# Kernel tuning notes

Measured on AMD Instinct MI355X. Metric: run time of the kernel, lower is better.

Reference implementation:

```python
import jax, jax.numpy as jnp
import numpy as np

D_MODEL = 512
D_STATE = 64
D_CONV = 4
EXPAND = 2
D_INNER = EXPAND * D_MODEL          # 1024
DT_RANK = (D_MODEL + 15) // 16      # 32 (ceil(d_model/16), standard Mamba)
B, L = 2, 1024
EPS = 1e-6


def setup_inputs() -> dict:
    key = jax.random.key(0)
    ks = jax.random.split(key, 12)
    s = 0.02
    p = {}
    p["x"] = jax.random.normal(ks[0], (B, L, D_MODEL), jnp.float32)
    # shared _Mamba params (share_dir=True)
    p["W_in"] = jax.random.normal(ks[1], (2 * D_INNER, D_MODEL), jnp.float32) * s
    p["conv_w"] = jax.random.normal(ks[2], (D_INNER, 1, D_CONV), jnp.float32) * s
    p["conv_b"] = jnp.zeros((D_INNER,), jnp.float32)
    p["W_xproj"] = jax.random.normal(ks[3], (DT_RANK + 2 * D_STATE, D_INNER), jnp.float32) * s
    p["W_dt"] = jax.random.normal(ks[4], (D_INNER, DT_RANK), jnp.float32) * s
    p["b_dt"] = jax.random.uniform(ks[5], (D_INNER,), jnp.float32, -4.0, -2.0)  # small dt after softplus
    p["A_log"] = jnp.log(jnp.broadcast_to(jnp.arange(1, D_STATE + 1, dtype=jnp.float32), (D_INNER, D_STATE)))
    p["Dskip"] = jnp.ones((D_INNER,), jnp.float32)
    p["W_out"] = jax.random.normal(ks[6], (D_MODEL, D_INNER), jnp.float32) * s
    # block params
    p["norm_in_w"] = jnp.ones((D_MODEL,), jnp.float32)
    p["fuse_W"] = jax.random.normal(ks[7], (2 * D_MODEL, 2 * D_MODEL), jnp.float32) * s
    p["fuse_b"] = jnp.zeros((2 * D_MODEL,), jnp.float32)
    p["ff_W1"] = jax.random.normal(ks[8], (4 * D_MODEL, D_MODEL), jnp.float32) * s
    p["ff_W2"] = jax.random.normal(ks[9], (D_MODEL, 4 * D_MODEL), jnp.float32) * s
    p["norm_out_w"] = jnp.ones((D_MODEL,), jnp.float32)
    return p


def _rmsnorm(x, w):
    x32 = x.astype(jnp.float32)
    var = jnp.mean(x32 * x32, axis=-1, keepdims=True)
    return (w * (x32 * jax.lax.rsqrt(var + EPS))).astype(x.dtype)


def _mamba(h, W_in, conv_w, conv_b, W_xproj, W_dt, b_dt, A_log, Dskip, W_out):
    # h: [B, L, D_MODEL]
    xz = jnp.einsum('bld,ed->ble', h, W_in)           # [B,L,2*D_INNER]
    u, z = jnp.split(xz, 2, axis=-1)
    # depthwise causal conv over time
    uc = jnp.transpose(u, (0, 2, 1))                  # [B,D_INNER,L]
    uc = jax.lax.conv_general_dilated(uc, conv_w, (1,), [(D_CONV - 1, 0)],
                                      feature_group_count=D_INNER)
    u = jax.nn.silu(jnp.transpose(uc, (0, 2, 1)) + conv_b)  # [B,L,D_INNER]
    x_dbl = jnp.einsum('bld,ed->ble', u, W_xproj)     # [B,L,DT_RANK+2N]
    dt = jax.nn.softplus(jnp.einsum('blr,dr->bld', x_dbl[..., :DT_RANK], W_dt) + b_dt)  # [B,L,D_INNER]
    Bm = x_dbl[..., DT_RANK:DT_RANK + D_STATE]        # [B,L,N]
    Cm = x_dbl[..., DT_RANK + D_STATE:]               # [B,L,N]
    A = -jnp.exp(A_log)                               # [D_INNER,N]

    def step(s, inp):
        dt_t, B_t, C_t, u_t = inp                     # [B,Din],[B,N],[B,N],[B,Din]
        dA = jnp.exp(dt_t[..., None] * A)             # [B,Din,N]
        s = s * dA + (dt_t * u_t)[..., None] * B_t[:, None, :]
        y_t = jnp.einsum('bdn,bn->bd', s, C_t)
        return s, y_t

    s0 = jnp.zeros((h.shape[0], D_INNER, D_STATE), h.dtype)
    xs = (jnp.moveaxis(dt, 1, 0), jnp.moveaxis(Bm, 1, 0),
          jnp.moveaxis(Cm, 1, 0), jnp.moveaxis(u, 1, 0))
    _, ys = jax.lax.scan(step, s0, xs)                # [L,B,D_INNER]
    y = jnp.moveaxis(ys, 0, 1) + u * Dskip
    return jnp.einsum('bld,ed->ble', y * jax.nn.silu(z), W_out)


def reference(x, W_in, conv_w, conv_b, W_xproj, W_dt, b_dt, A_log, Dskip, W_out,
              norm_in_w, fuse_W, fuse_b, ff_W1, ff_W2, norm_out_w):
    h = _rmsnorm(x, norm_in_w)
    mam = lambda t: _mamba(t, W_in, conv_w, conv_b, W_xproj, W_dt, b_dt, A_log, Dskip, W_out)
    hf = mam(h)
    hb = jnp.flip(mam(jnp.flip(h, axis=1)), axis=1)   # shared params (share_dir=True)
    hcat = jnp.concatenate([hf, hb], axis=-1)         # [B,L,2D]
    uv = jnp.einsum('ble,fe->blf', hcat, fuse_W) + fuse_b
    ug, vg = jnp.split(uv, 2, axis=-1)
    h = ug * jax.nn.sigmoid(vg)                        # GLU fuse
    ff = jnp.einsum('bld,fd->blf', jax.nn.silu(h), ff_W1)
    ff = jnp.einsum('blf,df->bld', jax.nn.silu(ff), ff_W2)
    y = x + ff                                         # dropout=0 (eval)
    return _rmsnorm(y, norm_out_w)
```

## Files before the change

### kernel.cpp

```cpp
#include <hip/hip_runtime.h>
#include <math.h>

#define L_SEQ 1024
#define NC 64
#define CL 16

typedef unsigned short ushort_t;
typedef __attribute__((ext_vector_type(8))) short bf16x8_t;
typedef __attribute__((ext_vector_type(4))) float f32x4_t;
typedef __attribute__((ext_vector_type(2))) float f32x2_t;

__device__ __forceinline__ float sigmoidf_(float x){ return 1.f/(1.f+__expf(-x)); }
__device__ __forceinline__ float siluf_(float x){ return x*sigmoidf_(x); }
__device__ __forceinline__ float softplusf_(float x){ return (x>20.f)?x:log1pf(__expf(x)); }
__device__ __forceinline__ ushort_t f2bf(float f){
  union { float f; unsigned u; } a; a.f = f;
  unsigned u = a.u;
  unsigned r = (u + 0x7fffu + ((u >> 16) & 1u)) >> 16;
  return (ushort_t)r;
}
__device__ __forceinline__ float bf2f(ushort_t v){
  union { unsigned u; float f; } a; a.u = ((unsigned)v) << 16; return a.f;
}
__device__ __forceinline__ ushort_t f2h(float f){
  union { _Float16 h; ushort_t u; } c; c.h = (_Float16)f; return c.u;
}
__device__ __forceinline__ float h2f(ushort_t u){
  union { ushort_t u; _Float16 h; } c; c.u = u; return (float)c.h;
}

__global__ __launch_bounds__(256) void cast_all_weights(
    ushort_t* __restrict__ dst,
    const float* __restrict__ W_in, const float* __restrict__ W_xproj,
    const float* __restrict__ W_dt, const float* __restrict__ W_out,
    const float* __restrict__ fuse_W, const float* __restrict__ ff_W1,
    const float* __restrict__ ff_W2)
{
  int i = blockIdx.x*256 + threadIdx.x;
  if (i >= 4947968) return;
  float v;
  if (i < 1048576) v = W_in[i];
  else if (i < 1245184) { int j = i-1048576; v = (j < 163840) ? W_xproj[j] : 0.f; }
  else if (i < 1277952) v = W_dt[i-1245184];
  else if (i < 1802240) v = W_out[i-1277952];
  else if (i < 2850816) v = fuse_W[i-1802240];
  else if (i < 3899392) v = ff_W1[i-2850816];
  else v = ff_W2[i-3899392];
  dst[i] = f2bf(v);
}

__global__ __launch_bounds__(256) void rmsnorm_kernel(
    float* __restrict__ outf, ushort_t* __restrict__ outb,
    const float* __restrict__ in, const float* __restrict__ res,
    const float* __restrict__ w)
{
  int row = blockIdx.x, tid = threadIdx.x;
  size_t base = (size_t)row*512;
  float v0 = in[base+tid], v1 = in[base+tid+256];
  if (res) { v0 += res[base+tid]; v1 += res[base+tid+256]; }
  float ss = v0*v0 + v1*v1;
  #pragma unroll
  for (int off=32; off>0; off>>=1) ss += __shfl_down(ss, off, 64);
  __shared__ float red[4];
  int wv = tid>>6, ln = tid&63;
  if (ln==0) red[wv]=ss;
  __syncthreads();
  float tot = red[0]+red[1]+red[2]+red[3];
  float sc = rsqrtf(tot*(1.f/512.f) + 1e-6f);
  float o0 = w[tid]*v0*sc, o1 = w[tid+256]*v1*sc;
  if (outb) { outb[base+tid] = f2bf(o0); outb[base+tid+256] = f2bf(o1); }
  else      { outf[base+tid] = o0;       outf[base+tid+256] = o1; }
}

template<int TM, int TN>
__global__ __launch_bounds__(256) void mfma_gemm(
    const ushort_t* __restrict__ A, int lda,
    const ushort_t* __restrict__ W, int ldw,
    float* __restrict__ Cf, ushort_t* __restrict__ Cb, int ldc,
    int N, int K, const float* __restrict__ bias, int act, int dsplit,
    ushort_t* __restrict__ Pr, ushort_t* __restrict__ Pdtu,
    const ushort_t* __restrict__ Pu)
{
  constexpr int BM = 32*TM, BN = 32*TN;
  constexpr int NSEG = (BM + BN) / 16;
  __shared__ ushort_t As[BM*32];
  __shared__ ushort_t Bs[BN*32];
  const int tid = threadIdx.x;
  const int wid = tid >> 6, lane = tid & 63;
  const int wm = (wid & 1) * (16*TM);
  const int wn = (wid >> 1) * (16*TN);
  const int row0 = blockIdx.y * BM;
  const int col0 = blockIdx.x * BN;
  const int qd = lane >> 4, lr = lane & 15;
  const int seg_row = lane >> 2;
  const int seg_col = (lane & 3) * 8;

  f32x4_t acc[TM][TN];
  #pragma unroll
  for (int i=0;i<TM;++i)
    #pragma unroll
    for (int j=0;j<TN;++j) acc[i][j] = (f32x4_t)(0.f);

  for (int k0 = 0; k0 < K; k0 += 32) {
    #pragma unroll
    for (int ss = 0; ss < NSEG/4; ++ss) {
      int s = wid + ss*4;
      bool isA = (s < BM/16);
      int r = isA ? s*16 : (s - BM/16)*16;
      const ushort_t* gp = isA
          ? (A + (size_t)(row0 + r + seg_row)*lda + k0 + seg_col)
          : (W + (size_t)(col0 + r + seg_row)*ldw + k0 + seg_col);
      ushort_t* lp = (isA ? As : Bs) + r*32;
      __builtin_amdgcn_global_load_lds(
          (const __attribute__((address_space(1))) void*)gp,
          (__attribute__((address_space(3))) void*)lp, 16, 0, 0);
    }
    __syncthreads();
    bf16x8_t af[TM], bfv[TN];
    #pragma unroll
    for (int mi=0; mi<TM; ++mi)
      af[mi] = *(const bf16x8_t*)(As + (wm + mi*16 + lr)*32 + qd*8);
    #pragma unroll
    for (int ni=0; ni<TN; ++ni)
      bfv[ni] = *(const bf16x8_t*)(Bs + (wn + ni*16 + lr)*32 + qd*8);
    #pragma unroll
    for (int mi=0; mi<TM; ++mi)
      #pragma unroll
      for (int ni=0; ni<TN; ++ni)
        acc[mi][ni] = __builtin_amdgcn_mfma_f32_16x16x32_bf16(af[mi], bfv[ni], acc[mi][ni], 0, 0, 0);
    __syncthreads();
  }

  #pragma unroll
  for (int ni=0; ni<TN; ++ni) {
    int col = col0 + wn + ni*16 + lr;
    if (col >= N) continue;
    float bv = bias ? bias[col] : 0.f;
    #pragma unroll
    for (int mi=0; mi<TM; ++mi) {
      #pragma unroll
      for (int r=0; r<4; ++r) {
        int row = row0 + wm + mi*16 + qd*4 + r;
        float v = acc[mi][ni][r] + bv;
        if (act == 1) v = softplusf_(v);
        else if (act == 2) v = siluf_(v);
        size_t off;
        if (dsplit && row >= 2048) off = (size_t)(row-2048)*ldc + 512 + col;
        else                       off = (size_t)row*ldc + col;
        if (Pr) {
          float uu = bf2f(Pu[off]);
          Pr[off]   = f2h(__expf(-v));
          Pdtu[off] = f2bf(v*uu);
        } else {
          if (Cf) Cf[off] = v;
          if (Cb) Cb[off] = f2bf(v);
        }
      }
    }
  }
}

__global__ __launch_bounds__(256) void conv_silu_kernel(
    ushort_t* __restrict__ ubf, const ushort_t* __restrict__ xzb,
    const float* __restrict__ conv_w, const float* __restrict__ conv_b)
{
  size_t gid = (size_t)blockIdx.x*256 + threadIdx.x;
  int d   = gid & 1023;
  int l   = (gid >> 10) & 1023;
  int b   = (gid >> 20) & 1;
  int dir = (int)(gid >> 21);
  const float4 wv = ((const float4*)conv_w)[d];
  const float wk[4] = {wv.x, wv.y, wv.z, wv.w};
  const ushort_t* xp = xzb + (size_t)b*L_SEQ*2048 + d;
  float acc = conv_b[d];
  if (dir == 0) {
    #pragma unroll
    for (int k=0;k<4;++k){ int ll=l-3+k; if(ll>=0) acc += bf2f(xp[(size_t)ll*2048])*wk[k]; }
  } else {
    #pragma unroll
    for (int k=0;k<4;++k){ int ll=l+3-k; if(ll<L_SEQ) acc += bf2f(xp[(size_t)ll*2048])*wk[k]; }
  }
  size_t oidx = (size_t)dir*2097152 + ((size_t)b*L_SEQ + l)*1024 + d;
  ubf[oidx] = f2bf(siluf_(acc));
}


__global__ __launch_bounds__(256) void scan_pass1(
    const ushort_t* __restrict__ rb, const ushort_t* __restrict__ dtub,
    const float* __restrict__ xdbl,
    float* __restrict__ prch, ushort_t* __restrict__ qbuf)
{
  __shared__ float bst[CL*64];
  int tid = threadIdx.x;
  int w = tid >> 6, lane = tid & 63;
  int dblk = blockIdx.x, c = blockIdx.y, sd = blockIdx.z;
  int b = sd>>1, dir = sd&1;
  int d = (dblk<<6) + lane;
  int n0 = w*16;
  size_t dbo = (size_t)dir*2097152 + (size_t)b*1048576;
  const ushort_t* rp  = rb   + dbo;
  const ushort_t* dup = dtub + dbo;
  const float* xd = xdbl + (size_t)dir*327680 + (size_t)b*163840;
  int l0c = c*CL;
  {
    int e = tid;
    int li = e >> 4, fo = (e & 15) << 2;
    int l = dir ? (L_SEQ-1-(l0c+li)) : (l0c+li);
    *(float4*)(bst + li*64 + fo) = *(const float4*)(xd + (size_t)l*160 + 32 + fo);
  }
  __syncthreads();
  f32x2_t s2[8];
  #pragma unroll
  for (int n=0;n<8;++n) s2[n]=(f32x2_t)(0.f);
  float pr = 1.f;
  int l0 = dir ? (L_SEQ-1-l0c) : l0c;
  float rv_n = h2f(rp[(size_t)l0*1024 + d]);
  float du_n = bf2f(dup[(size_t)l0*1024 + d]);
  #pragma unroll 1
  for (int i=0;i<CL;++i) {
    float rv = rv_n, du = du_n;
    if (i+1 < CL) {
      int l2 = dir ? (l0-i-1) : (l0+i+1);
      rv_n = h2f(rp[(size_t)l2*1024 + d]);
      du_n = bf2f(dup[(size_t)l2*1024 + d]);
    }
    const f32x2_t* B2 = (const f32x2_t*)(bst + i*64 + n0);
    pr *= rv;
    float r2 = rv*rv, r4 = r2*r2;
    float rs;
    if (w==0) rs = rv;
    else { float r8=r4*r4, r16=r8*r8;
           rs = (w==1)? r16*rv : (w==2)? r16*r16*rv : r16*r16*r16*rv; }
    f32x2_t c01 = {rs, rs*rv};
    f32x2_t c23 = {rs*r2, rs*r2*rv};
    f32x2_t r44 = {r4, r4};
    f32x2_t du2 = {du, du};
    #pragma unroll
    for (int jj=0;jj<4;++jj) {
      s2[2*jj+0] = s2[2*jj+0]*c01 + du2*B2[2*jj+0];
      s2[2*jj+1] = s2[2*jj+1]*c23 + du2*B2[2*jj+1];
      c01 *= r44; c23 *= r44;
    }
  }
  if (w==0) prch[((size_t)sd*NC + c)*1024 + d] = pr;
  ushort_t* qp = qbuf + ((size_t)(sd*NC + c)*64 + n0)*1024 + d;
  #pragma unroll
  for (int n=0;n<16;++n) qp[(size_t)n*1024] = f2bf(s2[n>>1][n&1]);
}

__global__ __launch_bounds__(256) void scan_pass2(
    const float* __restrict__ prch, ushort_t* __restrict__ qbuf)
{
  int gid = blockIdx.x*256 + threadIdx.x;
  int d  = gid & 1023;
  int n  = (gid >> 10) & 63;
  int sd = gid >> 16;
  float np1 = (float)(n+1);
  float s = 0.f;
  #pragma unroll 1
  for (int c=0;c<NC;++c) {
    size_t qidx = ((size_t)(sd*NC+c)*64 + n)*1024 + d;
    float qv = bf2f(qbuf[qidx]);
    float pr = prch[((size_t)sd*NC+c)*1024 + d];
    float P  = __expf(np1 * __logf(pr));
    qbuf[qidx] = f2bf(s);
    s = s*P + qv;
  }
}

__global__ __launch_bounds__(256) void scan_pass3(
    const ushort_t* __restrict__ rb, const ushort_t* __restrict__ dtub,
    const ushort_t* __restrict__ ub, const float* __restrict__ xdbl,
    const ushort_t* __restrict__ qbuf, const ushort_t* __restrict__ xzb,
    const float* __restrict__ Dskip, ushort_t* __restrict__ ycb)
{
  __shared__ float bcst[CL*128];
  __shared__ ushort_t ypart[4*CL*64];
  int tid = threadIdx.x;
  int w = tid >> 6, lane = tid & 63;
  int dblk = blockIdx.x, c = blockIdx.y, sd = blockIdx.z;
  int b = sd>>1, dir = sd&1;
  int d = (dblk<<6) + lane;
  int n0 = w*16;
  size_t dbo = (size_t)dir*2097152 + (size_t)b*1048576;
  const ushort_t* rp  = rb   + dbo;
  const ushort_t* dup = dtub + dbo;
  const ushort_t* up  = ub   + dbo;
  ushort_t* yp = ycb + dbo;
  const float* xd = xdbl + (size_t)dir*327680 + (size_t)b*163840;
  int l0c = c*CL;
  #pragma unroll
  for (int e = tid; e < CL*32; e += 256) {
    int li = e >> 5, fo = (e & 31) << 2;
    int l = dir ? (L_SEQ-1-(l0c+li)) : (l0c+li);
    *(float4*)(bcst + li*128 + fo) = *(const float4*)(xd + (size_t)l*160 + 32 + fo);
  }
  f32x2_t s2[8];
  const ushort_t* qp = qbuf + ((size_t)(sd*NC + c)*64 + n0)*1024 + d;
  #pragma unroll
  for (int n=0;n<16;++n) s2[n>>1][n&1] = bf2f(qp[(size_t)n*1024]);
  float Dv = (w==0) ? Dskip[d] : 0.f;
  int l0 = dir ? (L_SEQ-1-l0c) : l0c;
  float rv_n = h2f(rp[(size_t)l0*1024 + d]);
  float du_n = bf2f(dup[(size_t)l0*1024 + d]);
  float uv_n = (w==0) ? bf2f(up[(size_t)l0*1024 + d]) : 0.f;
  __syncthreads();
  #pragma unroll 1
  for (int i=0;i<CL;++i) {
    float rv = rv_n, du = du_n, uvv = uv_n;
    if (i+1 < CL) {
      int l2 = dir ? (l0-i-1) : (l0+i+1);
      rv_n = h2f(rp[(size_t)l2*1024 + d]);
      du_n = bf2f(dup[(size_t)l2*1024 + d]);
      if (w==0) uv_n = bf2f(up[(size_t)l2*1024 + d]);
    }
    const f32x2_t* B2 = (const f32x2_t*)(bcst + i*128 + n0);
    const f32x2_t* C2 = (const f32x2_t*)(bcst + i*128 + 64 + n0);
    float r2 = rv*rv, r4 = r2*r2;
    float rs;
    if (w==0) rs = rv;
    else { float r8=r4*r4, r16=r8*r8;
           rs = (w==1)? r16*rv : (w==2)? r16*r16*rv : r16*r16*r16*rv; }
    f32x2_t c01 = {rs, rs*rv};
    f32x2_t c23 = {rs*r2, rs*r2*rv};
    f32x2_t r44 = {r4, r4};
    f32x2_t du2 = {du, du};
    f32x2_t y01 = (f32x2_t)(0.f), y23 = (f32x2_t)(0.f);
    #pragma unroll
    for (int jj=0;jj<4;++jj) {
      s2[2*jj+0] = s2[2*jj+0]*c01 + du2*B2[2*jj+0];
      y01 = y01 + s2[2*jj+0]*C2[2*jj+0];
      s2[2*jj+1] = s2[2*jj+1]*c23 + du2*B2[2*jj+1];
      y23 = y23 + s2[2*jj+1]*C2[2*jj+1];
      c01 *= r44; c23 *= r44;
    }
    float yv = (y01[0]+y01[1])+(y23[0]+y23[1]) + uvv*Dv;
    ypart[(w*CL + i)*64 + lane] = f2bf(yv);
  }
  __syncthreads();
  #pragma unroll
  for (int k=0;k<CL/4;++k) {
    int i = w + 4*k;
    int l = dir ? (l0-i) : (l0+i);
    float y = bf2f(ypart[(0*CL + i)*64 + lane]) + bf2f(ypart[(1*CL + i)*64 + lane])
            + bf2f(ypart[(2*CL + i)*64 + lane]) + bf2f(ypart[(3*CL + i)*64 + lane]);
    float zv = bf2f(xzb[((size_t)b*L_SEQ + l)*2048 + 1024 + d]);
    yp[(size_t)l*1024 + d] = f2bf(y * siluf_(zv));
  }
}

__global__ __launch_bounds__(256) void glu_kernel(
    ushort_t* __restrict__ h2s, const float* __restrict__ uv)
{
  int gid = blockIdx.x*256 + threadIdx.x;
  int m = gid >> 9, j = gid & 511;
  float ug = uv[(size_t)m*1024 + j];
  float vg = uv[(size_t)m*1024 + 512 + j];
  float hv = ug * sigmoidf_(vg);
  h2s[gid] = f2bf(siluf_(hv));
}

extern "C" void kernel_launch(void* const* d_in, const int* in_sizes, int n_in,
                              void* d_out, int out_size, void* d_ws, size_t ws_size,
                              hipStream_t stream) {
  const float* x        = (const float*)d_in[0];
  const float* W_in     = (const float*)d_in[1];
  const float* conv_w   = (const float*)d_in[2];
  const float* conv_b   = (const float*)d_in[3];
  const float* W_xproj  = (const float*)d_in[4];
  const float* W_dt     = (const float*)d_in[5];
  const float* b_dt     = (const float*)d_in[6];
  const float* Dskip    = (const float*)d_in[8];
  const float* W_out    = (const float*)d_in[9];
  const float* norm_in_w  = (const float*)d_in[10];
  const float* fuse_W   = (const float*)d_in[11];
  const float* fuse_b   = (const float*)d_in[12];
  const float* ff_W1    = (const float*)d_in[13];
  const float* ff_W2    = (const float*)d_in[14];
  const float* norm_out_w = (const float*)d_in[15];
  float* out = (float*)d_out;

  float* ws = (float*)d_ws;
  ushort_t* xzb   = (ushort_t*)(ws + 0);
  ushort_t* ubf   = (ushort_t*)(ws + 2097152);
  float*    xdblf = ws + 4194304;
  ushort_t* xdblb = (ushort_t*)(ws + 4849664);
  ushort_t* rb    = (ushort_t*)(ws + 5177344);
  ushort_t* dtub  = (ushort_t*)(ws + 7274496);
  float*    prch  = ws + 9371648;
  ushort_t* qbuf  = (ushort_t*)(ws + 9633792);
  ushort_t* h_bf  = (ushort_t*)(ws + 9633792);
  ushort_t* wb    = (ushort_t*)(ws + 18022400);
  ushort_t* W_in_bf  = wb;
  ushort_t* W_xp_bf  = wb + 1048576;
  ushort_t* W_dt_bf  = wb + 1245184;
  ushort_t* W_out_bf = wb + 1277952;
  ushort_t* fuseW_bf = wb + 1802240;
  ushort_t* ffW1_bf  = wb + 2850816;
  ushort_t* ffW2_bf  = wb + 3899392;
  ushort_t* ycb  = ubf;
  ushort_t* hfhb = (ushort_t*)(ws + 5177344);
  float*    uvb  = ws + 0;
  ushort_t* h2s  = (ushort_t*)(ws + 2097152);
  ushort_t* ff1s = (ushort_t*)(ws + 9633792);
  float*    ff2  = ws + 7274496;

  cast_all_weights<<<19328, 256, 0, stream>>>(wb, W_in, W_xproj, W_dt, W_out,
                                              fuse_W, ff_W1, ff_W2);
  rmsnorm_kernel<<<2048, 256, 0, stream>>>(nullptr, h_bf, x, nullptr, norm_in_w);
  mfma_gemm<4,4><<<dim3(16,16), 256, 0, stream>>>(h_bf,512, W_in_bf,512,
      nullptr, xzb, 2048, 2048,512, nullptr,0,0, nullptr,nullptr,nullptr);
  conv_silu_kernel<<<16384, 256, 0, stream>>>(ubf, xzb, conv_w, conv_b);
  mfma_gemm<2,2><<<dim3(3,64), 256, 0, stream>>>(ubf,1024, W_xp_bf,1024,
      xdblf, xdblb, 160, 160,1024, nullptr,0,0, nullptr,nullptr,nullptr);
  mfma_gemm<2,2><<<dim3(16,64), 256, 0, stream>>>(xdblb,160, W_dt_bf,32,
      nullptr, nullptr, 1024, 1024,32, b_dt,1,0, rb, dtub, ubf);
  scan_pass1<<<dim3(16,NC,4), 256, 0, stream>>>(rb, dtub, xdblf, prch, qbuf);
  scan_pass2<<<1024, 256, 0, stream>>>(prch, qbuf);
  scan_pass3<<<dim3(16,NC,4), 256, 0, stream>>>(rb, dtub, ubf, xdblf, qbuf, xzb, Dskip, ycb);
  mfma_gemm<2,2><<<dim3(8,64), 256, 0, stream>>>(ycb,1024, W_out_bf,1024,
      nullptr, hfhb, 1024, 512,1024, nullptr,0,1, nullptr,nullptr,nullptr);
  mfma_gemm<2,2><<<dim3(16,32), 256, 0, stream>>>(hfhb,1024, fuseW_bf,1024,
      uvb, nullptr, 1024, 1024,1024, fuse_b,0,0, nullptr,nullptr,nullptr);
  glu_kernel<<<4096, 256, 0, stream>>>(h2s, uvb);
  mfma_gemm<4,4><<<dim3(16,16), 256, 0, stream>>>(h2s,512, ffW1_bf,512,
      nullptr, ff1s, 2048, 2048,512, nullptr,2,0, nullptr,nullptr,nullptr);
  mfma_gemm<2,2><<<dim3(8,32), 256, 0, stream>>>(ff1s,2048, ffW2_bf,2048,
      ff2, nullptr, 512, 512,2048, nullptr,0,0, nullptr,nullptr,nullptr);
  rmsnorm_kernel<<<2048, 256, 0, stream>>>(out, nullptr, ff2, x, norm_out_w);
}
```

Before: 402.3 us.

## Swizzle GEMM LDS layout, split-K ff_W2 GEMM, shrink tiles for big GEMMs

Applies an XOR swizzle to the LDS layout used by the MFMA GEMM so that fragment reads spread across banks instead of conflicting. The ff_W2 GEMM is split along K into two z-slices that write separate partial outputs, and the final rmsnorm sums both partials together with the residual. The W_in and ff_W1 GEMMs switch from 4x4 to 2x4 wave tiles to launch twice as many blocks. These trade some extra partial-sum memory traffic and lower per-block reuse for better occupancy and fewer LDS bank conflicts.

```diff
diff --git a/kernel.cpp b/kernel.cpp
--- a/kernel.cpp
+++ b/kernel.cpp
@@ -52,12 +52,13 @@
 __global__ __launch_bounds__(256) void rmsnorm_kernel(
     float* __restrict__ outf, ushort_t* __restrict__ outb,
     const float* __restrict__ in, const float* __restrict__ res,
-    const float* __restrict__ w)
+    const float* __restrict__ res2, const float* __restrict__ w)
 {
   int row = blockIdx.x, tid = threadIdx.x;
   size_t base = (size_t)row*512;
   float v0 = in[base+tid], v1 = in[base+tid+256];
-  if (res) { v0 += res[base+tid]; v1 += res[base+tid+256]; }
+  if (res)  { v0 += res[base+tid];  v1 += res[base+tid+256]; }
+  if (res2) { v0 += res2[base+tid]; v1 += res2[base+tid+256]; }
   float ss = v0*v0 + v1*v1;
   #pragma unroll
   for (int off=32; off>0; off>>=1) ss += __shfl_down(ss, off, 64);
@@ -79,7 +80,7 @@
     float* __restrict__ Cf, ushort_t* __restrict__ Cb, int ldc,
     int N, int K, const float* __restrict__ bias, int act, int dsplit,
     ushort_t* __restrict__ Pr, ushort_t* __restrict__ Pdtu,
-    const ushort_t* __restrict__ Pu)
+    const ushort_t* __restrict__ Pu, int kz_cstride)
 {
   constexpr int BM = 32*TM, BN = 32*TN;
   constexpr int NSEG = (BM + BN) / 16;
@@ -91,9 +92,14 @@
   const int wn = (wid >> 1) * (16*TN);
   const int row0 = blockIdx.y * BM;
   const int col0 = blockIdx.x * BN;
+  const int zz = blockIdx.z;
+  const int kbase = zz * K;
   const int qd = lane >> 4, lr = lane & 15;
   const int seg_row = lane >> 2;
-  const int seg_col = (lane & 3) * 8;
+  const int seg_swz = (seg_row & 3) ^ ((seg_row >> 2) & 3);
+  const int seg_col = ((lane & 3) ^ seg_swz) * 8;
+  const int rd_swz  = (lr & 3) ^ ((lr >> 2) & 3);
+  const int rd_off  = (qd ^ rd_swz) * 8;
 
   f32x4_t acc[TM][TN];
   #pragma unroll
@@ -108,8 +114,8 @@
       bool isA = (s < BM/16);
       int r = isA ? s*16 : (s - BM/16)*16;
       const ushort_t* gp = isA
-          ? (A + (size_t)(row0 + r + seg_row)*lda + k0 + seg_col)
-          : (W + (size_t)(col0 + r + seg_row)*ldw + k0 + seg_col);
+          ? (A + (size_t)(row0 + r + seg_row)*lda + kbase + k0 + seg_col)
+          : (W + (size_t)(col0 + r + seg_row)*ldw + kbase + k0 + seg_col);
       ushort_t* lp = (isA ? As : Bs) + r*32;
       __builtin_amdgcn_global_load_lds(
           (const __attribute__((address_space(1))) void*)gp,
@@ -119,10 +125,10 @@
     bf16x8_t af[TM], bfv[TN];
     #pragma unroll
     for (int mi=0; mi<TM; ++mi)
-      af[mi] = *(const bf16x8_t*)(As + (wm + mi*16 + lr)*32 + qd*8);
+      af[mi] = *(const bf16x8_t*)(As + (wm + mi*16 + lr)*32 + rd_off);
     #pragma unroll
     for (int ni=0; ni<TN; ++ni)
-      bfv[ni] = *(const bf16x8_t*)(Bs + (wn + ni*16 + lr)*32 + qd*8);
+      bfv[ni] = *(const bf16x8_t*)(Bs + (wn + ni*16 + lr)*32 + rd_off);
     #pragma unroll
     for (int mi=0; mi<TM; ++mi)
       #pragma unroll
@@ -147,6 +153,7 @@
         size_t off;
         if (dsplit && row >= 2048) off = (size_t)(row-2048)*ldc + 512 + col;
         else                       off = (size_t)row*ldc + col;
+        off += (size_t)zz * kz_cstride;
         if (Pr) {
           float uu = bf2f(Pu[off]);
           Pr[off]   = f2h(__expf(-v));
@@ -403,29 +410,29 @@
   float*    uvb  = ws + 0;
   ushort_t* h2s  = (ushort_t*)(ws + 2097152);
   ushort_t* ff1s = (ushort_t*)(ws + 9633792);
-  float*    ff2  = ws + 7274496;
+  float*    ff2p = ws + 7274496;
 
   cast_all_weights<<<19328, 256, 0, stream>>>(wb, W_in, W_xproj, W_dt, W_out,
                                               fuse_W, ff_W1, ff_W2);
-  rmsnorm_kernel<<<2048, 256, 0, stream>>>(nullptr, h_bf, x, nullptr, norm_in_w);
-  mfma_gemm<4,4><<<dim3(16,16), 256, 0, stream>>>(h_bf,512, W_in_bf,512,
-      nullptr, xzb, 2048, 2048,512, nullptr,0,0, nullptr,nullptr,nullptr);
+  rmsnorm_kernel<<<2048, 256, 0, stream>>>(nullptr, h_bf, x, nullptr, nullptr, norm_in_w);
+  mfma_gemm<2,4><<<dim3(16,32), 256, 0, stream>>>(h_bf,512, W_in_bf,512,
+      nullptr, xzb, 2048, 2048,512, nullptr,0,0, nullptr,nullptr,nullptr, 0);
   conv_silu_kernel<<<16384, 256, 0, stream>>>(ubf, xzb, conv_w, conv_b);
   mfma_gemm<2,2><<<dim3(3,64), 256, 0, stream>>>(ubf,1024, W_xp_bf,1024,
-      xdblf, xdblb, 160, 160,1024, nullptr,0,0, nullptr,nullptr,nullptr);
+      xdblf, xdblb, 160, 160,1024, nullptr,0,0, nullptr,nullptr,nullptr, 0);
   mfma_gemm<2,2><<<dim3(16,64), 256, 0, stream>>>(xdblb,160, W_dt_bf,32,
-      nullptr, nullptr, 1024, 1024,32, b_dt,1,0, rb, dtub, ubf);
+      nullptr, nullptr, 1024, 1024,32, b_dt,1,0, rb, dtub, ubf, 0);
   scan_pass1<<<dim3(16,NC,4), 256, 0, stream>>>(rb, dtub, xdblf, prch, qbuf);
   scan_pass2<<<1024, 256, 0, stream>>>(prch, qbuf);
   scan_pass3<<<dim3(16,NC,4), 256, 0, stream>>>(rb, dtub, ubf, xdblf, qbuf, xzb, Dskip, ycb);
   mfma_gemm<2,2><<<dim3(8,64), 256, 0, stream>>>(ycb,1024, W_out_bf,1024,
-      nullptr, hfhb, 1024, 512,1024, nullptr,0,1, nullptr,nullptr,nullptr);
+      nullptr, hfhb, 1024, 512,1024, nullptr,0,1, nullptr,nullptr,nullptr, 0);
   mfma_gemm<2,2><<<dim3(16,32), 256, 0, stream>>>(hfhb,1024, fuseW_bf,1024,
-      uvb, nullptr, 1024, 1024,1024, fuse_b,0,0, nullptr,nullptr,nullptr);
+      uvb, nullptr, 1024, 1024,1024, fuse_b,0,0, nullptr,nullptr,nullptr, 0);
   glu_kernel<<<4096, 256, 0, stream>>>(h2s, uvb);
-  mfma_gemm<4,4><<<dim3(16,16), 256, 0, stream>>>(h2s,512, ffW1_bf,512,
-      nullptr, ff1s, 2048, 2048,512, nullptr,2,0, nullptr,nullptr,nullptr);
-  mfma_gemm<2,2><<<dim3(8,32), 256, 0, stream>>>(ff1s,2048, ffW2_bf,2048,
-      ff2, nullptr, 512, 512,2048, nullptr,0,0, nullptr,nullptr,nullptr);
-  rmsnorm_kernel<<<2048, 256, 0, stream>>>(out, nullptr, ff2, x, norm_out_w);
-}
+  mfma_gemm<2,4><<<dim3(16,32), 256, 0, stream>>>(h2s,512, ffW1_bf,512,
+      nullptr, ff1s, 2048, 2048,512, nullptr,2,0, nullptr,nullptr,nullptr, 0);
+  mfma_gemm<2,2><<<dim3(8,32,2), 256, 0, stream>>>(ff1s,2048, ffW2_bf,2048,
+      ff2p, nullptr, 512, 512,1024, nullptr,0,0, nullptr,nullptr,nullptr, 1048576);
+  rmsnorm_kernel<<<2048, 256, 0, stream>>>(out, nullptr, ff2p, x, ff2p + 1048576, norm_out_w);
+}
```

Result: faster. 346.1 us (-14.0%).
